# Optimization experiments

Measured on AMD Instinct MI355X. Metric: run time of the kernel, lower is better.

Reference implementation:

```python
import jax, jax.numpy as jnp
import numpy as np

N_WIN = 7
DIM = 128
QK = 128
HEADS = 8
TOPK = 4


def _win(x, n_win):
    # (N, H, W, C) -> (N, n_win*n_win, h, w, C)
    N, H, W, C = x.shape
    h, w = H // n_win, W // n_win
    return x.reshape(N, n_win, h, n_win, w, C).transpose(0, 1, 3, 2, 4, 5).reshape(N, n_win * n_win, h, w, C)


def _unwin(x, n_win):
    # (N, p2, h, w, C) -> (N, H, W, C)
    N, p2, h, w, C = x.shape
    return x.reshape(N, n_win, n_win, h, w, C).transpose(0, 1, 3, 2, 4, 5).reshape(N, n_win * h, n_win * w, C)


def _dwconv(img_nhwc, k, b):
    # depthwise 3x3, SAME padding (LePE)
    x = img_nhwc.transpose(0, 3, 1, 2)
    y = jax.lax.conv_general_dilated(x, k, (1, 1), 'SAME',
                                     dimension_numbers=('NCHW', 'OIHW', 'NCHW'),
                                     feature_group_count=k.shape[0])
    y = y + b[None, :, None, None]
    return y.transpose(0, 2, 3, 1)


def _branch(xw, W, b):
    # xw: (N, p2, h, w, C); QKV linear + pixel/window-level views
    qkv = xw @ W + b
    q, kv = qkv[..., :QK], qkv[..., QK:]
    N, p2, h, w, _ = q.shape
    q_pix = q.reshape(N, p2, h * w, QK)
    kv_pix = kv.reshape(N, p2, h * w, QK + DIM)  # identity kv_down
    q_win = q.mean((2, 3))
    k_win = kv[..., :QK].mean((2, 3))
    return q_pix, kv_pix, q_win, k_win, kv


def _route(q_win, k_win, scale):
    # non-differentiable routing (detach) with Identity emb
    q = jax.lax.stop_gradient(q_win)
    k = jax.lax.stop_gradient(k_win)
    logit = (q * scale) @ k.transpose(0, 2, 1)  # (N, p2, p2)
    top_val, top_idx = jax.lax.top_k(logit, TOPK)
    r_weight = jax.nn.softmax(top_val, axis=-1)  # unused (mul_weight='none')
    return r_weight, top_idx


def _gather(kv_pix, idx):
    # kv_pix: (N, p2, w2, c), idx: (N, p2, K) -> (N, p2, K, w2, c)
    N = kv_pix.shape[0]
    bidx = jnp.arange(N)[:, None, None]
    return kv_pix[bidx, idx]


def _heads_q(q):
    # (N, p2, w2, m*c) -> (N, p2, m, w2, c)
    N, p2, w2, _ = q.shape
    return q.reshape(N, p2, w2, HEADS, -1).transpose(0, 1, 3, 2, 4)


def _heads_kv(kv):
    # (N, p2, K, w2, m*c) -> (N, p2, m, K*w2, c)
    N, p2, K, w2, _ = kv.shape
    return kv.reshape(N, p2, K, w2, HEADS, -1).transpose(0, 1, 4, 2, 3, 5).reshape(N, p2, HEADS, K * w2, -1)


def setup_inputs() -> dict:
    key = jax.random.key(0)
    ks = jax.random.split(key, 6)
    N, H, W = 8, 56, 56
    return {
        'x': jax.random.normal(ks[0], (N, H, W, DIM), jnp.float32),
        'y': jax.random.normal(ks[1], (N, H, W, DIM), jnp.float32),
        'w_qkv_x': jax.random.normal(ks[2], (DIM, 2 * QK + DIM), jnp.float32) * 0.02,
        'b_qkv_x': jnp.zeros((2 * QK + DIM,), jnp.float32),
        'w_qkv_y': jax.random.normal(ks[3], (DIM, 2 * QK + DIM), jnp.float32) * 0.02,
        'b_qkv_y': jnp.zeros((2 * QK + DIM,), jnp.float32),
        'w_lepe_x': jax.random.normal(ks[4], (DIM, 1, 3, 3), jnp.float32) * 0.1,
        'b_lepe_x': jnp.zeros((DIM,), jnp.float32),
        'w_lepe_y': jax.random.normal(ks[5], (DIM, 1, 3, 3), jnp.float32) * 0.1,
        'b_lepe_y': jnp.zeros((DIM,), jnp.float32),
    }


def reference(x, y, w_qkv_x, b_qkv_x, w_qkv_y, b_qkv_y, w_lepe_x, b_lepe_x, w_lepe_y, b_lepe_y):
    scale = QK ** (-0.5)
    N, H, W, C = x.shape
    h, w = H // N_WIN, W // N_WIN
    xw = _win(x, N_WIN)
    yw = _win(y, N_WIN)

    qx_pix, kvx_pix, qx_win, kx_win, kvx = _branch(xw, w_qkv_x, b_qkv_x)
    qy_pix, kvy_pix, qy_win, ky_win, kvy = _branch(yw, w_qkv_y, b_qkv_y)

    lepe_x = _dwconv(_unwin(kvx[..., QK:], N_WIN), w_lepe_x, b_lepe_x)
    lepe_y = _dwconv(_unwin(kvy[..., QK:], N_WIN), w_lepe_y, b_lepe_y)

    _, rx_idx = _route(qx_win, kx_win, scale)
    _, ry_idx = _route(qy_win, ky_win, scale)

    kvx_sel = _gather(kvx_pix, rx_idx)  # (N, p2, K, w2, QK+DIM)
    kvy_sel = _gather(kvy_pix, ry_idx)

    kx_sel, vx_sel = _heads_kv(kvx_sel[..., :QK]), _heads_kv(kvx_sel[..., QK:])
    ky_sel, vy_sel = _heads_kv(kvy_sel[..., :QK]), _heads_kv(kvy_sel[..., QK:])
    qx = _heads_q(qx_pix)
    qy = _heads_q(qy_pix)

    attn_x = jax.nn.softmax(jnp.einsum('bpmqc,bpmkc->bpmqk', qx * scale, kx_sel), axis=-1)
    attn_y = jax.nn.softmax(jnp.einsum('bpmqc,bpmkc->bpmqk', qy * scale, ky_sel), axis=-1)

    # cross attention: x-output uses y's attention weights on x's values, and vice versa
    out_x = jnp.einsum('bpmqk,bpmkc->bpmqc', attn_y, vx_sel)
    out_y = jnp.einsum('bpmqk,bpmkc->bpmqc', attn_x, vy_sel)

    p2 = N_WIN * N_WIN
    out_x = out_x.transpose(0, 1, 3, 2, 4).reshape(N, p2, h, w, DIM)
    out_y = out_y.transpose(0, 1, 3, 2, 4).reshape(N, p2, h, w, DIM)
    out_x = _unwin(out_x, N_WIN) + lepe_x
    out_y = _unwin(out_y, N_WIN) + lepe_y
    return (out_x, out_y)
```

## Files before the change

### kernel.cpp

```cpp
#include <hip/hip_runtime.h>

#define HWD 56
#define NWIN 7
#define P2 49
#define CIN 128
#define COUT 384
#define NB 8
#define SCALE 0.08838834764831843f

typedef __attribute__((ext_vector_type(8))) short bf16x8;
typedef __attribute__((ext_vector_type(4))) float f32x4;
typedef __attribute__((ext_vector_type(8))) unsigned short u16x8;
typedef unsigned short ushort_t;

__device__ inline unsigned short f2bf(float f) {
  unsigned int u = __float_as_uint(f);
  unsigned int r = (u + 0x7fffu + ((u >> 16) & 1u)) >> 16;
  return (unsigned short)r;
}
__device__ inline float bf2f(unsigned short b) {
  return __uint_as_float(((unsigned int)b) << 16);
}

#define KIDX(k) ((k) * 24 + (((k) >> 3) << 3))

__global__ __launch_bounds__(256) void meanproj_kernel(
    const float* __restrict__ xin, const float* __restrict__ yin,
    const float* __restrict__ Wx, const float* __restrict__ Bx,
    const float* __restrict__ Wy, const float* __restrict__ By,
    float* __restrict__ qwx, float* __restrict__ kwx,
    float* __restrict__ qwy, float* __restrict__ kwy)
{
  const int p = blockIdx.x, n = blockIdx.y, br = blockIdx.z;
  const float* X  = br ? yin : xin;
  const float* W  = br ? Wy  : Wx;
  const float* Bv = br ? By  : Bx;
  float* qw = br ? qwy : qwx;
  float* kw = br ? kwy : kwx;

  __shared__ float sm[2][128];
  __shared__ float mxs[128];
  const int t = threadIdx.x;
  const int wr = p / NWIN, wc = p % NWIN;
  const int ch = t & 127, half = t >> 7;

  float s = 0.f;
#pragma unroll 4
  for (int i = 0; i < 32; ++i) {
    int pix = half * 32 + i;
    int a = wr * 8 + (pix >> 3), b = wc * 8 + (pix & 7);
    s += X[(((size_t)n * HWD + a) * HWD + b) * CIN + ch];
  }
  sm[half][ch] = s;
  __syncthreads();
  if (t < 128) mxs[t] = (sm[0][t] + sm[1][t]) * (1.f / 64.f);
  __syncthreads();

  float acc = Bv[t];
#pragma unroll 8
  for (int k = 0; k < 128; ++k) acc = fmaf(mxs[k], W[(size_t)k * COUT + t], acc);
  if (t < 128) qw[(n * P2 + p) * 128 + t] = acc;
  else         kw[(n * P2 + p) * 128 + (t - 128)] = acc;
}

__global__ __launch_bounds__(256) void route_kernel(
    const float* __restrict__ qwx, const float* __restrict__ kwx,
    const float* __restrict__ qwy, const float* __restrict__ kwy,
    int* __restrict__ idxx, int* __restrict__ idxy)
{
  const int br = blockIdx.x, n = blockIdx.y;
  const float* qw = br ? qwy : qwx;
  const float* kw = br ? kwy : kwx;
  int* idx = br ? idxy : idxx;

  __shared__ float qs[P2][128];
  __shared__ float ks[P2][128];
  __shared__ float ls[P2][52];
  const int t = threadIdx.x;
  for (int e = t; e < P2 * 128; e += 256) {
    qs[e >> 7][e & 127] = qw[(size_t)n * P2 * 128 + e];
    ks[e >> 7][e & 127] = kw[(size_t)n * P2 * 128 + e];
  }
  __syncthreads();
  for (int pair = t; pair < P2 * P2; pair += 256) {
    int r = pair / P2, j = pair % P2;
    float d = 0.f;
#pragma unroll
    for (int c4 = 0; c4 < 32; ++c4) {
      float4 a = *(const float4*)&qs[r][c4 * 4];
      float4 b = *(const float4*)&ks[j][c4 * 4];
      d = fmaf(a.x, b.x, d); d = fmaf(a.y, b.y, d);
      d = fmaf(a.z, b.z, d); d = fmaf(a.w, b.w, d);
    }
    ls[r][j] = d;
  }
  __syncthreads();
  if (t < P2) {
    int ch[4];
    for (int s = 0; s < 4; ++s) {
      float best = -1e30f; int bi = 0;
      for (int j = 0; j < P2; ++j) {
        bool taken = false;
        for (int u = 0; u < s; ++u) taken = taken || (ch[u] == j);
        if (!taken && ls[t][j] > best) { best = ls[t][j]; bi = j; }
      }
      ch[s] = bi;
      idx[((size_t)n * P2 + t) * 4 + s] = bi;
    }
  }
}

#define AS 136
__global__ __launch_bounds__(256) void qkv_gemm_kernel(
    const float* __restrict__ xin, const float* __restrict__ yin,
    const float* __restrict__ Wx, const float* __restrict__ Bx,
    const float* __restrict__ Wy, const float* __restrict__ By,
    ushort_t* __restrict__ qkvx, ushort_t* __restrict__ qkvy)
{
  const int mt = blockIdx.x, nt = blockIdx.y, br = blockIdx.z;
  const float* X  = br ? yin : xin;
  const float* W  = br ? Wy  : Wx;
  const float* Bv = br ? By  : Bx;
  ushort_t* out = br ? qkvy : qkvx;

  __shared__ ushort_t a_s[128 * AS];
  __shared__ ushort_t b_s[128 * AS];

  const int t = threadIdx.x;

#pragma unroll
  for (int it = 0; it < 16; ++it) {
    int tok = it * 8 + (t >> 5);
    int ch4 = (t & 31) * 4;
    int gw = mt * 2 + (tok >> 6);
    int n = gw / P2, p = gw % P2;
    int pix = tok & 63;
    int a = (p / NWIN) * 8 + (pix >> 3), b = (p % NWIN) * 8 + (pix & 7);
    float4 v = *(const float4*)&X[(((size_t)n * HWD + a) * HWD + b) * CIN + ch4];
    ushort4 o = {f2bf(v.x), f2bf(v.y), f2bf(v.z), f2bf(v.w)};
    *(ushort4*)&a_s[tok * AS + ch4] = o;
  }
#pragma unroll
  for (int it = 0; it < 16; ++it) {
    int k = it * 8 + (t >> 5);
    int c4 = (t & 31) * 4;
    float4 v = *(const float4*)&W[(size_t)k * COUT + nt * 128 + c4];
    b_s[(c4 + 0) * AS + k] = f2bf(v.x);
    b_s[(c4 + 1) * AS + k] = f2bf(v.y);
    b_s[(c4 + 2) * AS + k] = f2bf(v.z);
    b_s[(c4 + 3) * AS + k] = f2bf(v.w);
  }
  __syncthreads();

  const int wv = t >> 6, wm = wv >> 1, wn = wv & 1;
  const int lane = t & 63, qd = lane >> 4, m16 = lane & 15;

  f32x4 acc[4][4];
#pragma unroll
  for (int i = 0; i < 4; ++i)
#pragma unroll
    for (int j = 0; j < 4; ++j) acc[i][j] = (f32x4){0.f, 0.f, 0.f, 0.f};

#pragma unroll
  for (int ks = 0; ks < 4; ++ks) {
    bf16x8 af[4], bfr[4];
#pragma unroll
    for (int fi = 0; fi < 4; ++fi)
      af[fi] = *(const bf16x8*)&a_s[(wm * 64 + fi * 16 + m16) * AS + ks * 32 + qd * 8];
#pragma unroll
    for (int fj = 0; fj < 4; ++fj)
      bfr[fj] = *(const bf16x8*)&b_s[(wn * 64 + fj * 16 + m16) * AS + ks * 32 + qd * 8];
#pragma unroll
    for (int fi = 0; fi < 4; ++fi)
#pragma unroll
      for (int fj = 0; fj < 4; ++fj)
        acc[fi][fj] = __builtin_amdgcn_mfma_f32_16x16x32_bf16(af[fi], bfr[fj], acc[fi][fj], 0, 0, 0);
  }

  const int gw = mt * 2 + wm;
#pragma unroll
  for (int fj = 0; fj < 4; ++fj) {
    int chb = nt * 128 + wn * 64 + fj * 16 + m16;
    float bias = Bv[chb];
#pragma unroll
    for (int fi = 0; fi < 4; ++fi) {
      int pixb = fi * 16 + qd * 4;
      ushort4 st = {f2bf(acc[fi][fj][0] + bias), f2bf(acc[fi][fj][1] + bias),
                    f2bf(acc[fi][fj][2] + bias), f2bf(acc[fi][fj][3] + bias)};
      *(ushort4*)&out[((size_t)gw * COUT + chb) * 64 + pixb] = st;
    }
  }
}

__global__ __launch_bounds__(256) void attn_kernel(
    const ushort_t* __restrict__ qkvx, const ushort_t* __restrict__ qkvy,
    const int* __restrict__ idxx, const int* __restrict__ idxy,
    const float* __restrict__ wlx, const float* __restrict__ blx,
    const float* __restrict__ wly, const float* __restrict__ bly,
    float* __restrict__ dout)
{
  const int p = blockIdx.x, n = blockIdx.y, z = blockIdx.z;
  const int h = z >> 1, dir = z & 1;
  const ushort_t* qkvQ = dir ? qkvy : qkvx;
  const ushort_t* qkvV = dir ? qkvx : qkvy;
  const int* idxK = dir ? idxy : idxx;
  const int* idxV = dir ? idxx : idxy;
  const float* wl = dir ? wlx : wly;
  const float* bl = dir ? blx : bly;
  const size_t OUTHALF = (size_t)NB * HWD * HWD * CIN;
  float* outp = dout + (dir ? 0 : OUTHALF);

  __shared__ ushort_t kb[6400];
  __shared__ ushort_t vt[16 * 264];
  __shared__ ushort_t qb[1600];
  __shared__ int widx[8];

  const int t = threadIdx.x;
  if (t < 8) widx[t] = (t < 4) ? idxK[((size_t)n * P2 + p) * 4 + t]
                               : idxV[((size_t)n * P2 + p) * 4 + (t - 4)];
  __syncthreads();

  const int wv = t >> 6, r = t & 63;

  {
    int ch2 = r >> 3, g = r & 7, pixg = g * 8;
    const ushort_t* src = qkvQ + ((size_t)(n * P2 + widx[wv]) * COUT + 128 + h * 16 + 2 * ch2) * 64 + pixg;
    u16x8 v0 = *(const u16x8*)src;
    u16x8 v1 = *(const u16x8*)(src + 64);
#pragma unroll
    for (int i = 0; i < 8; ++i) {
      int key = wv * 64 + pixg + i;
      *(unsigned int*)&kb[KIDX(key) + 2 * ch2] = (unsigned int)v0[i] | ((unsigned int)v1[i] << 16);
    }
  }
  {
    int ch_l = r >> 2, pixg = (r & 3) * 16;
    const ushort_t* src = qkvV + ((size_t)(n * P2 + widx[4 + wv]) * COUT + 256 + h * 16 + ch_l) * 64 + pixg;
    *(u16x8*)&vt[ch_l * 264 + wv * 64 + pixg] = *(const u16x8*)src;
    *(u16x8*)&vt[ch_l * 264 + wv * 64 + pixg + 8] = *(const u16x8*)(src + 8);
  }
  if (t < 64) {
    int ch2 = t >> 3, g = t & 7, pixg = g * 8;
    const ushort_t* src = qkvQ + ((size_t)(n * P2 + p) * COUT + h * 16 + 2 * ch2) * 64 + pixg;
    u16x8 v0 = *(const u16x8*)src;
    u16x8 v1 = *(const u16x8*)(src + 64);
#pragma unroll
    for (int i = 0; i < 8; ++i)
      *(unsigned int*)&qb[KIDX(pixg + i) + 2 * ch2] = (unsigned int)v0[i] | ((unsigned int)v1[i] << 16);
  }
  __syncthreads();

  const int qd = (t & 63) >> 4, m16 = t & 15;

  bf16x8 qf = (bf16x8)(short)0;
  if (qd < 2) qf = *(const bf16x8*)&qb[KIDX(wv * 16 + m16) + qd * 8];

  f32x4 oacc = {0.f, 0.f, 0.f, 0.f};
  float mrun = -1e30f, lrun = 0.f;
  const f32x4 zf = {0.f, 0.f, 0.f, 0.f};

  for (int c = 0; c < 8; ++c) {
    bf16x8 kf0 = (bf16x8)(short)0, kf1 = (bf16x8)(short)0;
    if (qd < 2) {
      kf0 = *(const bf16x8*)&kb[KIDX(c * 32 + m16) + qd * 8];
      kf1 = *(const bf16x8*)&kb[KIDX(c * 32 + 16 + m16) + qd * 8];
    }
    f32x4 s0 = __builtin_amdgcn_mfma_f32_16x16x32_bf16(kf0, qf, zf, 0, 0, 0);
    f32x4 s1 = __builtin_amdgcn_mfma_f32_16x16x32_bf16(kf1, qf, zf, 0, 0, 0);

    float mc = -1e30f;
#pragma unroll
    for (int rr = 0; rr < 4; ++rr) {
      s0[rr] *= SCALE; s1[rr] *= SCALE;
      mc = fmaxf(mc, fmaxf(s0[rr], s1[rr]));
    }
    mc = fmaxf(mc, __shfl_xor(mc, 16));
    mc = fmaxf(mc, __shfl_xor(mc, 32));
    float mn = fmaxf(mrun, mc);
    float alpha = __expf(mrun - mn);
    mrun = mn;
    float p0[4], p1[4], rs = 0.f;
#pragma unroll
    for (int rr = 0; rr < 4; ++rr) {
      p0[rr] = __expf(s0[rr] - mn);
      p1[rr] = __expf(s1[rr] - mn);
      rs += p0[rr] + p1[rr];
    }
    rs += __shfl_xor(rs, 16);
    rs += __shfl_xor(rs, 32);
    lrun = lrun * alpha + rs;
#pragma unroll
    for (int rr = 0; rr < 4; ++rr) oacc[rr] *= alpha;

    int pk[4];
#pragma unroll
    for (int rr = 0; rr < 4; ++rr)
      pk[rr] = (int)((unsigned int)f2bf(p0[rr]) | ((unsigned int)f2bf(p1[rr]) << 16));
    u16x8 pfu;
#pragma unroll
    for (int j = 0; j < 8; ++j) {
      int srcl = (((qd & 1) * 2 + (j >> 2)) << 4) + m16;
      int w = __shfl(pk[j & 3], srcl);
      pfu[j] = (qd < 2) ? (unsigned short)(w & 0xffff) : (unsigned short)((unsigned)w >> 16);
    }
    bf16x8 vtf = *(const bf16x8*)&vt[m16 * 264 + c * 32 + qd * 8];
    oacc = __builtin_amdgcn_mfma_f32_16x16x32_bf16(vtf, *(bf16x8*)&pfu, oacc, 0, 0, 0);
  }

  const float inv = 1.f / lrun;
  const int wr = p / NWIN, wc = p % NWIN;
  const int pix = wv * 16 + m16;
  const int ga = wr * 8 + (pix >> 3), gb = wc * 8 + (pix & 7);
  const int ch0 = h * 16 + qd * 4;

  float wlv[4][9], lep[4];
#pragma unroll
  for (int rr = 0; rr < 4; ++rr) {
    lep[rr] = bl[ch0 + rr];
#pragma unroll
    for (int tap = 0; tap < 9; ++tap) wlv[rr][tap] = wl[(ch0 + rr) * 9 + tap];
  }
#pragma unroll
  for (int di = 0; di < 3; ++di) {
    int aa = ga + di - 1;
    if ((unsigned)aa < (unsigned)HWD) {
#pragma unroll
      for (int dj = 0; dj < 3; ++dj) {
        int bb = gb + dj - 1;
        if ((unsigned)bb < (unsigned)HWD) {
          int pp = (aa >> 3) * NWIN + (bb >> 3);
          int pix2 = ((aa & 7) << 3) + (bb & 7);
          const ushort_t* vsrc = qkvV + ((size_t)(n * P2 + pp) * COUT + 256 + ch0) * 64 + pix2;
#pragma unroll
          for (int rr = 0; rr < 4; ++rr)
            lep[rr] = fmaf(bf2f(vsrc[rr * 64]), wlv[rr][di * 3 + dj], lep[rr]);
        }
      }
    }
  }

  float4 o = {oacc[0] * inv + lep[0], oacc[1] * inv + lep[1],
              oacc[2] * inv + lep[2], oacc[3] * inv + lep[3]};
  *(float4*)&outp[(((size_t)n * HWD + ga) * HWD + gb) * CIN + ch0] = o;
}

extern "C" void kernel_launch(void* const* d_in, const int* in_sizes, int n_in,
                              void* d_out, int out_size, void* d_ws, size_t ws_size,
                              hipStream_t stream) {
  const float* x        = (const float*)d_in[0];
  const float* y        = (const float*)d_in[1];
  const float* w_qkv_x  = (const float*)d_in[2];
  const float* b_qkv_x  = (const float*)d_in[3];
  const float* w_qkv_y  = (const float*)d_in[4];
  const float* b_qkv_y  = (const float*)d_in[5];
  const float* w_lepe_x = (const float*)d_in[6];
  const float* b_lepe_x = (const float*)d_in[7];
  const float* w_lepe_y = (const float*)d_in[8];
  const float* b_lepe_y = (const float*)d_in[9];
  float* out = (float*)d_out;

  const size_t qkv_sz = (size_t)NB * P2 * 64 * COUT;
  const size_t win_sz = (size_t)NB * P2 * 128;
  ushort_t* qkvx = (ushort_t*)d_ws;
  ushort_t* qkvy = qkvx + qkv_sz;
  float* qwx = (float*)(qkvy + qkv_sz);
  float* kwx = qwx + win_sz;
  float* qwy = kwx + win_sz;
  float* kwy = qwy + win_sz;
  int* idxx = (int*)(kwy + win_sz);
  int* idxy = idxx + NB * P2 * 4;

  meanproj_kernel<<<dim3(P2, NB, 2), 256, 0, stream>>>(
      x, y, w_qkv_x, b_qkv_x, w_qkv_y, b_qkv_y, qwx, kwx, qwy, kwy);
  route_kernel<<<dim3(2, NB), 256, 0, stream>>>(qwx, kwx, qwy, kwy, idxx, idxy);
  qkv_gemm_kernel<<<dim3(196, 3, 2), 256, 0, stream>>>(
      x, y, w_qkv_x, b_qkv_x, w_qkv_y, b_qkv_y, qkvx, qkvy);
  attn_kernel<<<dim3(P2, NB, 16), 256, 0, stream>>>(
      qkvx, qkvy, idxx, idxy, w_lepe_x, b_lepe_x, w_lepe_y, b_lepe_y, out);
}
```

Baseline: 237.5 us.

## Pre-window inputs to bf16, token-major QKV layout, halo-staged LePE in attention

The mean-projection kernel now also writes a windowed bf16 copy of the inputs, and a new small kernel pre-transposes the weights to bf16. The QKV GEMM therefore does plain vector copies into shared memory and writes its output token-major with the attention scale folded into q. The attention kernel loads K/Q/V rows contiguously, computes the softmax in one pass over all scores instead of an online update, and computes LePE from a halo tile in shared memory instead of scattered global reads. This adds an extra kernel launch and an extra bf16 round trip of the inputs through memory.

```diff
diff --git a/kernel.cpp b/kernel.cpp
--- a/kernel.cpp
+++ b/kernel.cpp
@@ -22,12 +22,11 @@
   return __uint_as_float(((unsigned int)b) << 16);
 }
 
-#define KIDX(k) ((k) * 24 + (((k) >> 3) << 3))
-
 __global__ __launch_bounds__(256) void meanproj_kernel(
     const float* __restrict__ xin, const float* __restrict__ yin,
     const float* __restrict__ Wx, const float* __restrict__ Bx,
     const float* __restrict__ Wy, const float* __restrict__ By,
+    ushort_t* __restrict__ xbfx, ushort_t* __restrict__ xbfy,
     float* __restrict__ qwx, float* __restrict__ kwx,
     float* __restrict__ qwy, float* __restrict__ kwy)
 {
@@ -35,6 +34,7 @@
   const float* X  = br ? yin : xin;
   const float* W  = br ? Wy  : Wx;
   const float* Bv = br ? By  : Bx;
+  ushort_t* xb = (br ? xbfy : xbfx) + (size_t)(n * P2 + p) * 64 * CIN;
   float* qw = br ? qwy : qwx;
   float* kw = br ? kwy : kwx;
 
@@ -49,7 +49,9 @@
   for (int i = 0; i < 32; ++i) {
     int pix = half * 32 + i;
     int a = wr * 8 + (pix >> 3), b = wc * 8 + (pix & 7);
-    s += X[(((size_t)n * HWD + a) * HWD + b) * CIN + ch];
+    float v = X[(((size_t)n * HWD + a) * HWD + b) * CIN + ch];
+    s += v;
+    xb[pix * CIN + ch] = f2bf(v);
   }
   sm[half][ch] = s;
   __syncthreads();
@@ -61,6 +63,22 @@
   for (int k = 0; k < 128; ++k) acc = fmaf(mxs[k], W[(size_t)k * COUT + t], acc);
   if (t < 128) qw[(n * P2 + p) * 128 + t] = acc;
   else         kw[(n * P2 + p) * 128 + (t - 128)] = acc;
+}
+
+__global__ __launch_bounds__(128) void wt_kernel(
+    const float* __restrict__ Wx, const float* __restrict__ Wy,
+    ushort_t* __restrict__ Wtx, ushort_t* __restrict__ Wty)
+{
+  const int br = blockIdx.y;
+  const float* W = br ? Wy : Wx;
+  ushort_t* Wt = br ? Wty : Wtx;
+  const int c = blockIdx.x * 128 + threadIdx.x;
+  for (int k8 = 0; k8 < 128; k8 += 8) {
+    u16x8 buf;
+#pragma unroll
+    for (int i = 0; i < 8; ++i) buf[i] = f2bf(W[(size_t)(k8 + i) * COUT + c]);
+    *(u16x8*)&Wt[(size_t)c * 128 + k8] = buf;
+  }
 }
 
 __global__ __launch_bounds__(256) void route_kernel(
@@ -112,43 +130,27 @@
 
 #define AS 136
 __global__ __launch_bounds__(256) void qkv_gemm_kernel(
-    const float* __restrict__ xin, const float* __restrict__ yin,
-    const float* __restrict__ Wx, const float* __restrict__ Bx,
-    const float* __restrict__ Wy, const float* __restrict__ By,
+    const ushort_t* __restrict__ xbfx, const ushort_t* __restrict__ xbfy,
+    const ushort_t* __restrict__ Wtx, const ushort_t* __restrict__ Wty,
+    const float* __restrict__ Bx, const float* __restrict__ By,
     ushort_t* __restrict__ qkvx, ushort_t* __restrict__ qkvy)
 {
   const int mt = blockIdx.x, nt = blockIdx.y, br = blockIdx.z;
-  const float* X  = br ? yin : xin;
-  const float* W  = br ? Wy  : Wx;
-  const float* Bv = br ? By  : Bx;
+  const ushort_t* Xb = br ? xbfy : xbfx;
+  const ushort_t* Wt = br ? Wty : Wtx;
+  const float* Bv = br ? By : Bx;
   ushort_t* out = br ? qkvy : qkvx;
 
   __shared__ ushort_t a_s[128 * AS];
   __shared__ ushort_t b_s[128 * AS];
 
   const int t = threadIdx.x;
-
-#pragma unroll
-  for (int it = 0; it < 16; ++it) {
-    int tok = it * 8 + (t >> 5);
-    int ch4 = (t & 31) * 4;
-    int gw = mt * 2 + (tok >> 6);
-    int n = gw / P2, p = gw % P2;
-    int pix = tok & 63;
-    int a = (p / NWIN) * 8 + (pix >> 3), b = (p % NWIN) * 8 + (pix & 7);
-    float4 v = *(const float4*)&X[(((size_t)n * HWD + a) * HWD + b) * CIN + ch4];
-    ushort4 o = {f2bf(v.x), f2bf(v.y), f2bf(v.z), f2bf(v.w)};
-    *(ushort4*)&a_s[tok * AS + ch4] = o;
-  }
-#pragma unroll
-  for (int it = 0; it < 16; ++it) {
-    int k = it * 8 + (t >> 5);
-    int c4 = (t & 31) * 4;
-    float4 v = *(const float4*)&W[(size_t)k * COUT + nt * 128 + c4];
-    b_s[(c4 + 0) * AS + k] = f2bf(v.x);
-    b_s[(c4 + 1) * AS + k] = f2bf(v.y);
-    b_s[(c4 + 2) * AS + k] = f2bf(v.z);
-    b_s[(c4 + 3) * AS + k] = f2bf(v.w);
+#pragma unroll
+  for (int it = 0; it < 8; ++it) {
+    int row = it * 16 + (t >> 4);
+    int e8 = (t & 15) * 8;
+    *(u16x8*)&a_s[row * AS + e8] = *(const u16x8*)&Xb[((size_t)mt * 128 + row) * 128 + e8];
+    *(u16x8*)&b_s[row * AS + e8] = *(const u16x8*)&Wt[((size_t)nt * 128 + row) * 128 + e8];
   }
   __syncthreads();
 
@@ -174,24 +176,25 @@
     for (int fi = 0; fi < 4; ++fi)
 #pragma unroll
       for (int fj = 0; fj < 4; ++fj)
-        acc[fi][fj] = __builtin_amdgcn_mfma_f32_16x16x32_bf16(af[fi], bfr[fj], acc[fi][fj], 0, 0, 0);
-  }
-
-  const int gw = mt * 2 + wm;
+        acc[fi][fj] = __builtin_amdgcn_mfma_f32_16x16x32_bf16(bfr[fj], af[fi], acc[fi][fj], 0, 0, 0);
+  }
+
+  const float scl = (nt == 0) ? SCALE : 1.0f;
 #pragma unroll
   for (int fj = 0; fj < 4; ++fj) {
-    int chb = nt * 128 + wn * 64 + fj * 16 + m16;
-    float bias = Bv[chb];
+    int chb = nt * 128 + wn * 64 + fj * 16 + qd * 4;
+    float4 b4 = *(const float4*)&Bv[chb];
 #pragma unroll
     for (int fi = 0; fi < 4; ++fi) {
-      int pixb = fi * 16 + qd * 4;
-      ushort4 st = {f2bf(acc[fi][fj][0] + bias), f2bf(acc[fi][fj][1] + bias),
-                    f2bf(acc[fi][fj][2] + bias), f2bf(acc[fi][fj][3] + bias)};
-      *(ushort4*)&out[((size_t)gw * COUT + chb) * 64 + pixb] = st;
-    }
-  }
-}
-
+      int tok = wm * 64 + fi * 16 + m16;
+      ushort4 st = {f2bf((acc[fi][fj][0] + b4.x) * scl), f2bf((acc[fi][fj][1] + b4.y) * scl),
+                    f2bf((acc[fi][fj][2] + b4.z) * scl), f2bf((acc[fi][fj][3] + b4.w) * scl)};
+      *(ushort4*)&out[((size_t)mt * 128 + tok) * COUT + chb] = st;
+    }
+  }
+}
+
+#define KR 24
 __global__ __launch_bounds__(256) void attn_kernel(
     const ushort_t* __restrict__ qkvx, const ushort_t* __restrict__ qkvy,
     const int* __restrict__ idxx, const int* __restrict__ idxy,
@@ -210,92 +213,109 @@
   const size_t OUTHALF = (size_t)NB * HWD * HWD * CIN;
   float* outp = dout + (dir ? 0 : OUTHALF);
 
-  __shared__ ushort_t kb[6400];
+  __shared__ ushort_t kb[256 * KR];
+  __shared__ ushort_t qb[64 * KR];
   __shared__ ushort_t vt[16 * 264];
-  __shared__ ushort_t qb[1600];
-  __shared__ int widx[8];
+  __shared__ float halo[100 * 20];
+  __shared__ float wls[160];
 
   const int t = threadIdx.x;
-  if (t < 8) widx[t] = (t < 4) ? idxK[((size_t)n * P2 + p) * 4 + t]
-                               : idxV[((size_t)n * P2 + p) * 4 + (t - 4)];
-  __syncthreads();
-
   const int wv = t >> 6, r = t & 63;
+  const int wr = p / NWIN, wc = p % NWIN;
+
+  const int kwin = idxK[((size_t)n * P2 + p) * 4 + wv];
+  const int vwin = idxV[((size_t)n * P2 + p) * 4 + wv];
 
   {
-    int ch2 = r >> 3, g = r & 7, pixg = g * 8;
-    const ushort_t* src = qkvQ + ((size_t)(n * P2 + widx[wv]) * COUT + 128 + h * 16 + 2 * ch2) * 64 + pixg;
+    const ushort_t* src = qkvQ + ((size_t)(n * P2 + kwin) * 64 + r) * COUT + 128 + h * 16;
+    *(u16x8*)&kb[t * KR] = *(const u16x8*)src;
+    *(u16x8*)&kb[t * KR + 8] = *(const u16x8*)(src + 8);
+  }
+  if (t < 64) {
+    const ushort_t* src = qkvQ + ((size_t)(n * P2 + p) * 64 + t) * COUT + h * 16;
+    *(u16x8*)&qb[t * KR] = *(const u16x8*)src;
+    *(u16x8*)&qb[t * KR + 8] = *(const u16x8*)(src + 8);
+  }
+  {
+    const ushort_t* src = qkvV + ((size_t)(n * P2 + vwin) * 64 + r) * COUT + 256 + h * 16;
     u16x8 v0 = *(const u16x8*)src;
-    u16x8 v1 = *(const u16x8*)(src + 64);
-#pragma unroll
-    for (int i = 0; i < 8; ++i) {
-      int key = wv * 64 + pixg + i;
-      *(unsigned int*)&kb[KIDX(key) + 2 * ch2] = (unsigned int)v0[i] | ((unsigned int)v1[i] << 16);
-    }
-  }
-  {
-    int ch_l = r >> 2, pixg = (r & 3) * 16;
-    const ushort_t* src = qkvV + ((size_t)(n * P2 + widx[4 + wv]) * COUT + 256 + h * 16 + ch_l) * 64 + pixg;
-    *(u16x8*)&vt[ch_l * 264 + wv * 64 + pixg] = *(const u16x8*)src;
-    *(u16x8*)&vt[ch_l * 264 + wv * 64 + pixg + 8] = *(const u16x8*)(src + 8);
-  }
-  if (t < 64) {
-    int ch2 = t >> 3, g = t & 7, pixg = g * 8;
-    const ushort_t* src = qkvQ + ((size_t)(n * P2 + p) * COUT + h * 16 + 2 * ch2) * 64 + pixg;
-    u16x8 v0 = *(const u16x8*)src;
-    u16x8 v1 = *(const u16x8*)(src + 64);
-#pragma unroll
-    for (int i = 0; i < 8; ++i)
-      *(unsigned int*)&qb[KIDX(pixg + i) + 2 * ch2] = (unsigned int)v0[i] | ((unsigned int)v1[i] << 16);
-  }
-  __syncthreads();
-
-  const int qd = (t & 63) >> 4, m16 = t & 15;
+    u16x8 v1 = *(const u16x8*)(src + 8);
+#pragma unroll
+    for (int c = 0; c < 8; ++c) {
+      vt[c * 264 + wv * 64 + r] = v0[c];
+      vt[(c + 8) * 264 + wv * 64 + r] = v1[c];
+    }
+  }
+  if (t < 200) {
+    int hp = t >> 1, hf = t & 1;
+    int A = wr * 8 - 1 + (int)((unsigned)hp / 10u);
+    int B = wc * 8 - 1 + (int)((unsigned)hp % 10u);
+    f32x4 f0 = {0.f, 0.f, 0.f, 0.f}, f1 = {0.f, 0.f, 0.f, 0.f};
+    if ((unsigned)A < (unsigned)HWD && (unsigned)B < (unsigned)HWD) {
+      int gw = (A >> 3) * NWIN + (B >> 3);
+      int pix = (A & 7) * 8 + (B & 7);
+      u16x8 vv = *(const u16x8*)(qkvV + ((size_t)(n * P2 + gw) * 64 + pix) * COUT + 256 + h * 16 + hf * 8);
+      f0[0] = bf2f(vv[0]); f0[1] = bf2f(vv[1]); f0[2] = bf2f(vv[2]); f0[3] = bf2f(vv[3]);
+      f1[0] = bf2f(vv[4]); f1[1] = bf2f(vv[5]); f1[2] = bf2f(vv[6]); f1[3] = bf2f(vv[7]);
+    }
+    *(f32x4*)&halo[hp * 20 + hf * 8] = f0;
+    *(f32x4*)&halo[hp * 20 + hf * 8 + 4] = f1;
+  }
+  if (t < 160) {
+    int row = t >> 4, c = t & 15;
+    wls[t] = (row < 9) ? wl[(h * 16 + c) * 9 + row] : bl[h * 16 + c];
+  }
+  __syncthreads();
+
+  const int qd = r >> 4, m16 = r & 15;
+  const f32x4 zf = {0.f, 0.f, 0.f, 0.f};
 
   bf16x8 qf = (bf16x8)(short)0;
-  if (qd < 2) qf = *(const bf16x8*)&qb[KIDX(wv * 16 + m16) + qd * 8];
-
-  f32x4 oacc = {0.f, 0.f, 0.f, 0.f};
-  float mrun = -1e30f, lrun = 0.f;
-  const f32x4 zf = {0.f, 0.f, 0.f, 0.f};
-
+  if (qd < 2) qf = *(const bf16x8*)&qb[(wv * 16 + m16) * KR + qd * 8];
+
+  f32x4 s[8][2];
+#pragma unroll
   for (int c = 0; c < 8; ++c) {
     bf16x8 kf0 = (bf16x8)(short)0, kf1 = (bf16x8)(short)0;
     if (qd < 2) {
-      kf0 = *(const bf16x8*)&kb[KIDX(c * 32 + m16) + qd * 8];
-      kf1 = *(const bf16x8*)&kb[KIDX(c * 32 + 16 + m16) + qd * 8];
-    }
-    f32x4 s0 = __builtin_amdgcn_mfma_f32_16x16x32_bf16(kf0, qf, zf, 0, 0, 0);
-    f32x4 s1 = __builtin_amdgcn_mfma_f32_16x16x32_bf16(kf1, qf, zf, 0, 0, 0);
-
-    float mc = -1e30f;
-#pragma unroll
-    for (int rr = 0; rr < 4; ++rr) {
-      s0[rr] *= SCALE; s1[rr] *= SCALE;
-      mc = fmaxf(mc, fmaxf(s0[rr], s1[rr]));
-    }
-    mc = fmaxf(mc, __shfl_xor(mc, 16));
-    mc = fmaxf(mc, __shfl_xor(mc, 32));
-    float mn = fmaxf(mrun, mc);
-    float alpha = __expf(mrun - mn);
-    mrun = mn;
-    float p0[4], p1[4], rs = 0.f;
-#pragma unroll
-    for (int rr = 0; rr < 4; ++rr) {
-      p0[rr] = __expf(s0[rr] - mn);
-      p1[rr] = __expf(s1[rr] - mn);
-      rs += p0[rr] + p1[rr];
-    }
-    rs += __shfl_xor(rs, 16);
-    rs += __shfl_xor(rs, 32);
-    lrun = lrun * alpha + rs;
-#pragma unroll
-    for (int rr = 0; rr < 4; ++rr) oacc[rr] *= alpha;
-
+      kf0 = *(const bf16x8*)&kb[(c * 32 + m16) * KR + qd * 8];
+      kf1 = *(const bf16x8*)&kb[(c * 32 + 16 + m16) * KR + qd * 8];
+    }
+    s[c][0] = __builtin_amdgcn_mfma_f32_16x16x32_bf16(kf0, qf, zf, 0, 0, 0);
+    s[c][1] = __builtin_amdgcn_mfma_f32_16x16x32_bf16(kf1, qf, zf, 0, 0, 0);
+  }
+
+  float m = -1e30f;
+#pragma unroll
+  for (int c = 0; c < 8; ++c)
+#pragma unroll
+    for (int hh = 0; hh < 2; ++hh)
+#pragma unroll
+      for (int rr = 0; rr < 4; ++rr) m = fmaxf(m, s[c][hh][rr]);
+  m = fmaxf(m, __shfl_xor(m, 16));
+  m = fmaxf(m, __shfl_xor(m, 32));
+  float l = 0.f;
+#pragma unroll
+  for (int c = 0; c < 8; ++c)
+#pragma unroll
+    for (int hh = 0; hh < 2; ++hh)
+#pragma unroll
+      for (int rr = 0; rr < 4; ++rr) {
+        float e = __expf(s[c][hh][rr] - m);
+        s[c][hh][rr] = e;
+        l += e;
+      }
+  l += __shfl_xor(l, 16);
+  l += __shfl_xor(l, 32);
+  const float inv = 1.f / l;
+
+  f32x4 oacc = {0.f, 0.f, 0.f, 0.f};
+#pragma unroll
+  for (int c = 0; c < 8; ++c) {
     int pk[4];
 #pragma unroll
     for (int rr = 0; rr < 4; ++rr)
-      pk[rr] = (int)((unsigned int)f2bf(p0[rr]) | ((unsigned int)f2bf(p1[rr]) << 16));
+      pk[rr] = (int)((unsigned int)f2bf(s[c][0][rr]) | ((unsigned int)f2bf(s[c][1][rr]) << 16));
     u16x8 pfu;
 #pragma unroll
     for (int j = 0; j < 8; ++j) {
@@ -307,41 +327,24 @@
     oacc = __builtin_amdgcn_mfma_f32_16x16x32_bf16(vtf, *(bf16x8*)&pfu, oacc, 0, 0, 0);
   }
 
-  const float inv = 1.f / lrun;
-  const int wr = p / NWIN, wc = p % NWIN;
   const int pix = wv * 16 + m16;
-  const int ga = wr * 8 + (pix >> 3), gb = wc * 8 + (pix & 7);
-  const int ch0 = h * 16 + qd * 4;
-
-  float wlv[4][9], lep[4];
-#pragma unroll
-  for (int rr = 0; rr < 4; ++rr) {
-    lep[rr] = bl[ch0 + rr];
-#pragma unroll
-    for (int tap = 0; tap < 9; ++tap) wlv[rr][tap] = wl[(ch0 + rr) * 9 + tap];
-  }
-#pragma unroll
-  for (int di = 0; di < 3; ++di) {
-    int aa = ga + di - 1;
-    if ((unsigned)aa < (unsigned)HWD) {
-#pragma unroll
-      for (int dj = 0; dj < 3; ++dj) {
-        int bb = gb + dj - 1;
-        if ((unsigned)bb < (unsigned)HWD) {
-          int pp = (aa >> 3) * NWIN + (bb >> 3);
-          int pix2 = ((aa & 7) << 3) + (bb & 7);
-          const ushort_t* vsrc = qkvV + ((size_t)(n * P2 + pp) * COUT + 256 + ch0) * 64 + pix2;
-#pragma unroll
-          for (int rr = 0; rr < 4; ++rr)
-            lep[rr] = fmaf(bf2f(vsrc[rr * 64]), wlv[rr][di * 3 + dj], lep[rr]);
-        }
-      }
-    }
-  }
-
+  const int pa = pix >> 3, pb = pix & 7;
+
+  f32x4 lep = *(const f32x4*)&wls[144 + qd * 4];
+#pragma unroll
+  for (int di = 0; di < 3; ++di)
+#pragma unroll
+    for (int dj = 0; dj < 3; ++dj) {
+      f32x4 hv = *(const f32x4*)&halo[((pa + di) * 10 + pb + dj) * 20 + qd * 4];
+      f32x4 wt4 = *(const f32x4*)&wls[(di * 3 + dj) * 16 + qd * 4];
+#pragma unroll
+      for (int rr = 0; rr < 4; ++rr) lep[rr] = fmaf(hv[rr], wt4[rr], lep[rr]);
+    }
+
+  const int ga = wr * 8 + pa, gb = wc * 8 + pb;
   float4 o = {oacc[0] * inv + lep[0], oacc[1] * inv + lep[1],
               oacc[2] * inv + lep[2], oacc[3] * inv + lep[3]};
-  *(float4*)&outp[(((size_t)n * HWD + ga) * HWD + gb) * CIN + ch0] = o;
+  *(float4*)&outp[(((size_t)n * HWD + ga) * HWD + gb) * CIN + h * 16 + qd * 4] = o;
 }
 
 extern "C" void kernel_launch(void* const* d_in, const int* in_sizes, int n_in,
@@ -360,10 +363,17 @@
   float* out = (float*)d_out;
 
   const size_t qkv_sz = (size_t)NB * P2 * 64 * COUT;
+  const size_t xbf_sz = (size_t)NB * P2 * 64 * CIN;
+  const size_t wt_sz  = (size_t)COUT * CIN;
   const size_t win_sz = (size_t)NB * P2 * 128;
+
   ushort_t* qkvx = (ushort_t*)d_ws;
   ushort_t* qkvy = qkvx + qkv_sz;
-  float* qwx = (float*)(qkvy + qkv_sz);
+  ushort_t* xbfx = qkvy + qkv_sz;
+  ushort_t* xbfy = xbfx + xbf_sz;
+  ushort_t* Wtx  = xbfy + xbf_sz;
+  ushort_t* Wty  = Wtx + wt_sz;
+  float* qwx = (float*)(Wty + wt_sz);
   float* kwx = qwx + win_sz;
   float* qwy = kwx + win_sz;
   float* kwy = qwy + win_sz;
@@ -371,10 +381,11 @@
   int* idxy = idxx + NB * P2 * 4;
 
   meanproj_kernel<<<dim3(P2, NB, 2), 256, 0, stream>>>(
-      x, y, w_qkv_x, b_qkv_x, w_qkv_y, b_qkv_y, qwx, kwx, qwy, kwy);
+      x, y, w_qkv_x, b_qkv_x, w_qkv_y, b_qkv_y, xbfx, xbfy, qwx, kwx, qwy, kwy);
+  wt_kernel<<<dim3(3, 2), 128, 0, stream>>>(w_qkv_x, w_qkv_y, Wtx, Wty);
   route_kernel<<<dim3(2, NB), 256, 0, stream>>>(qwx, kwx, qwy, kwy, idxx, idxy);
   qkv_gemm_kernel<<<dim3(196, 3, 2), 256, 0, stream>>>(
-      x, y, w_qkv_x, b_qkv_x, w_qkv_y, b_qkv_y, qkvx, qkvy);
+      xbfx, xbfy, Wtx, Wty, b_qkv_x, b_qkv_y, qkvx, qkvy);
   attn_kernel<<<dim3(P2, NB, 16), 256, 0, stream>>>(
       qkvx, qkvy, idxx, idxy, w_lepe_x, b_lepe_x, w_lepe_y, b_lepe_y, out);
 }
```

Result: slower. 244.7 us (+3.0%).
